# Performance work log

Measured on AMD Instinct MI355X. Metric: run time of the kernel, lower is better.

The kernel has to match this reference:

```python
import jax, jax.numpy as jnp
import numpy as np
from jax import lax

K2 = 3                 # support_kernel_size
TARGET_OCC = 0.5
OCC_W = 10.0
ITERS = 10             # flood-fill iterations
THRESH = 0.5
STEEP = 20.0

# 6-neighbor 3D cross kernel (plus-shaped), shape [O=1, I=1, 3, 3, 3]
_cross_np = np.zeros((1, 1, 3, 3, 3), dtype=np.float32)
for dz, dy, dx in [(0, 1, 1), (2, 1, 1), (1, 0, 1), (1, 2, 1), (1, 1, 0), (1, 1, 2)]:
    _cross_np[0, 0, dz, dy, dx] = 1.0


def _conv3d(x, k, pad):
    # x: [B, C, D, H, W], k: [O, I, kd, kh, kw]
    return lax.conv_general_dilated(
        x, k, window_strides=(1, 1, 1), padding=pad,
        dimension_numbers=('NCDHW', 'OIDHW', 'NCDHW'))


def setup_inputs() -> dict:
    key = jax.random.key(0)
    voxel_grid = jax.random.uniform(key, (4, 1, 128, 128, 128), dtype=jnp.float32)
    return {"voxel_grid": voxel_grid}


def reference(voxel_grid):
    B, C, D, H, W = voxel_grid.shape
    N = B * D * H * W
    dt = voxel_grid.dtype

    # ---- overhang score: vectorized over all z-slices at once ----
    # per-slice conv2d(3x3 ones) == conv3d with kernel depth 1
    k2 = jnp.ones((1, 1, 1, K2, K2), dt)
    below = voxel_grid[:, :, :-1]          # [B,1,D-1,H,W]
    curr = voxel_grid[:, :, 1:]
    below_support = _conv3d(below, k2, ((0, 0), (1, 1), (1, 1)))
    support_ratio = below_support / (K2 * K2)
    overhang = (curr * (1.0 - support_ratio)).sum() / N

    # ---- surface area score ----
    k3 = jnp.ones((1, 1, 3, 3, 3), dt)
    neighbor_solid = _conv3d(voxel_grid, k3, ((1, 1), (1, 1), (1, 1)))
    surface_term = neighbor_solid.sum() / 27.0 / N

    occupancy = voxel_grid.sum() / N
    occupancy_penalty = OCC_W * (occupancy - TARGET_OCC) ** 2

    # differentiable flood-fill (diff_find_enclosed_voids)
    seed = jnp.zeros_like(voxel_grid).at[:, :, 5, 5, 5].set(1.0)
    cross = jnp.asarray(_cross_np, dt)
    not_solid = 1.0 - voxel_grid

    def body(i, mask):
        c = _conv3d(mask, cross, ((1, 1), (1, 1), (1, 1)))
        act = jax.nn.sigmoid(STEEP * (c - THRESH))
        return jnp.maximum(mask, act) * not_solid

    enclosed = lax.fori_loop(0, ITERS, body, seed)
    resin_trap_penalty = 100.0 * enclosed.sum() / N

    surface_score = surface_term - resin_trap_penalty - occupancy_penalty
    return overhang, surface_score
```

## Files before the change

kernel.cpp:

```cpp
#include <hip/hip_runtime.h>

#define HW    (128*128)
#define DHW   (128*128*128)
#define NTOT  (4*DHW)
#define NBLK  2048

__device__ __forceinline__ float sigf(float x){ return 1.0f/(1.0f+__expf(-x)); }
__device__ __forceinline__ float4 ld4(const float* p){ return *(const float4*)p; }


__global__ __launch_bounds__(256, 4) void mega_k(
    const float* __restrict__ v, float* __restrict__ p_occ,
    float* __restrict__ p_surf, float* __restrict__ p_over,
    float* __restrict__ p_trap)
{
    __shared__ float4 smem4[1445];
    __shared__ float sred[16];
    float* smem = (float*)smem4;

    const int bid = blockIdx.x;
    const int tid = threadIdx.x;
    const float4 zero4 = make_float4(0,0,0,0);

    if (bid < 4) {
        const int b = bid;
        const size_t gb = (size_t)b * DHW;
        const int ty = tid & 15, tz = tid >> 4;
        const float a_lo = sigf(-10.0f), a_hi = sigf(10.0f);
        #define M(zz,yy) (smem + (((zz)*17 + (yy))*20))

        float m[16], nv[16];
        {
            const float* rv = v + gb + ((size_t)tz*128 + ty)*128;
            int dzy = abs(tz-5) + abs(ty-5);
            #pragma unroll
            for (int q = 0; q < 4; ++q) {
                int x4 = 4*q;
                float4 a = ld4(rv + x4);
                nv[x4+0]=1.f-a.x; nv[x4+1]=1.f-a.y; nv[x4+2]=1.f-a.z; nv[x4+3]=1.f-a.w;
                int d0=dzy+abs(x4+0-5), d1=dzy+abs(x4+1-5);
                int d2=dzy+abs(x4+2-5), d3=dzy+abs(x4+3-5);
                m[x4+0] = ((d0==0)?1.f:((d0==1)?a_hi:a_lo)) * nv[x4+0];
                m[x4+1] = ((d1==0)?1.f:((d1==1)?a_hi:a_lo)) * nv[x4+1];
                m[x4+2] = ((d2==0)?1.f:((d2==1)?a_hi:a_lo)) * nv[x4+2];
                m[x4+3] = ((d3==0)?1.f:((d3==1)?a_hi:a_lo)) * nv[x4+3];
                *(float4*)(M(tz,ty) + x4) = make_float4(m[x4+0],m[x4+1],m[x4+2],m[x4+3]);
            }
        }
        const float xrE = a_lo * (1.f - v[gb + ((size_t)tz*128 + ty)*128 + 16]);
        {
            int a = tid >> 4, e = tid & 15;
            M(16,a)[e] = a_lo * (1.f - v[gb + ((size_t)16*128 + a)*128 + e]);
            M(a,16)[e] = a_lo * (1.f - v[gb + ((size_t)a*128 + 16)*128 + e]);
        }
        __syncthreads();

        for (int it = 0; it < 9; ++it) {
            const float* YM = M(tz,ty-1);
            const float* YP = M(tz,ty+1);
            const float* ZM = M(tz-1,ty);
            const float* ZP = M(tz+1,ty);
            float nm[16];
            #pragma unroll
            for (int q = 0; q < 4; ++q) {
                int x4 = 4*q;
                float4 ym = (ty > 0) ? *(const float4*)(YM + x4) : zero4;
                float4 yp = *(const float4*)(YP + x4);
                float4 zm = (tz > 0) ? *(const float4*)(ZM + x4) : zero4;
                float4 zp = *(const float4*)(ZP + x4);
                float xl = (q == 0) ? 0.f : m[x4-1];
                float xr = (q == 3) ? xrE : m[x4+4];
                float s0 = xl      + m[x4+1] + ym.x + yp.x + zm.x + zp.x;
                float s1 = m[x4+0] + m[x4+2] + ym.y + yp.y + zm.y + zp.y;
                float s2 = m[x4+1] + m[x4+3] + ym.z + yp.z + zm.z + zp.z;
                float s3 = m[x4+2] + xr      + ym.w + yp.w + zm.w + zp.w;
                nm[x4+0] = fmaxf(m[x4+0], sigf(20.f*s0 - 10.f)) * nv[x4+0];
                nm[x4+1] = fmaxf(m[x4+1], sigf(20.f*s1 - 10.f)) * nv[x4+1];
                nm[x4+2] = fmaxf(m[x4+2], sigf(20.f*s2 - 10.f)) * nv[x4+2];
                nm[x4+3] = fmaxf(m[x4+3], sigf(20.f*s3 - 10.f)) * nv[x4+3];
            }
            __syncthreads();
            float* W = M(tz,ty);
            #pragma unroll
            for (int q = 0; q < 4; ++q) {
                int x4 = 4*q;
                *(float4*)(W + x4) = make_float4(nm[x4+0],nm[x4+1],nm[x4+2],nm[x4+3]);
                m[x4+0]=nm[x4+0]; m[x4+1]=nm[x4+1]; m[x4+2]=nm[x4+2]; m[x4+3]=nm[x4+3];
            }
            __syncthreads();
        }

        float d = 0.f;
        #pragma unroll
        for (int x = 0; x < 16; ++x) d += m[x] - a_lo * nv[x];
        #pragma unroll
        for (int o = 32; o; o >>= 1) d += __shfl_down(d, o, 64);
        int lane = tid & 63, wid = tid >> 6;
        if (lane == 0) sred[wid] = d;
        __syncthreads();
        if (tid == 0) p_trap[b] = sred[0] + sred[1] + sred[2] + sred[3];
        #undef M
    } else {
        const int rid = bid - 4;
        const int b   = rid >> 9;
        const int rem = rid & 511;
        const int z0  = (rem >> 4) * 4;
        const int y0  = (rem & 15) * 8;
        const int tx  = tid & 31, ty = tid >> 5;
        const int x4  = tx * 4;
        const int y   = y0 + ty;
        const size_t gb = (size_t)b * DHW;
        #define PB(p,r) (smem + ((p)*1320 + (r)*132))

        float occ = 0.f, surf = 0.f, over = 0.f;

        if (z0 >= 1) {
            const float* bp = v + gb + (size_t)(z0-1)*HW;
            for (int i = tid; i < 320; i += 256) {
                int r = i >> 5, xq = i & 31, xi = xq*4;
                int gy = y0 - 1 + r;
                float4 q = ((unsigned)gy <= 127u) ? ld4(bp + gy*128 + xi) : zero4;
                float ql = __shfl_up(q.w, 1);   if (xq == 0)  ql = 0.f;
                float qr = __shfl_down(q.x, 1); if (xq == 31) qr = 0.f;
                *(float4*)(PB(0,r) + xi) =
                    make_float4(ql+q.x+q.y, q.x+q.y+q.z, q.y+q.z+q.w, q.z+q.w+qr);
            }
        }
        __syncthreads();

        const float wy = (y==0 || y==127) ? 2.f : 3.f;
        const float wx0 = (x4==0)   ? 2.f : 3.f;
        const float wx3 = (x4==124) ? 2.f : 3.f;
        const float inv9 = 1.f/9.f;

        int pb = 0;
        for (int s = 0; s < 4; ++s) {
            const int z = z0 + s;
            const float* cp = v + gb + (size_t)z*HW;
            float4 val = ld4(cp + y*128 + x4);

            occ += val.x + val.y + val.z + val.w;
            float wz = (z==0 || z==127) ? 2.f : 3.f;
            surf += wz*wy*(wx0*val.x + 3.f*val.y + 3.f*val.z + wx3*val.w);

            if (z >= 1) {
                float4 a = *(const float4*)(PB(pb, ty)   + x4);
                float4 c = *(const float4*)(PB(pb, ty+1) + x4);
                float4 d = *(const float4*)(PB(pb, ty+2) + x4);
                float4 S = make_float4(a.x+c.x+d.x, a.y+c.y+d.y,
                                       a.z+c.z+d.z, a.w+c.w+d.w);
                over += val.x*(1.f - S.x*inv9) + val.y*(1.f - S.y*inv9)
                      + val.z*(1.f - S.z*inv9) + val.w*(1.f - S.w*inv9);
            }

            if (s < 3) {
                float ql = __shfl_up(val.w, 1);   if (tx == 0)  ql = 0.f;
                float qr = __shfl_down(val.x, 1); if (tx == 31) qr = 0.f;
                *(float4*)(PB(pb^1, ty+1) + x4) =
                    make_float4(ql+val.x+val.y, val.x+val.y+val.z,
                                val.y+val.z+val.w, val.z+val.w+qr);
                if (tid < 64) {
                    int h = tid >> 5, xq = tid & 31, xi = xq*4;
                    int gy = h ? (y0 + 8) : (y0 - 1);
                    float4 q = ((unsigned)gy <= 127u) ? ld4(cp + gy*128 + xi) : zero4;
                    float hl = __shfl_up(q.w, 1);   if (xq == 0)  hl = 0.f;
                    float hr = __shfl_down(q.x, 1); if (xq == 31) hr = 0.f;
                    *(float4*)(PB(pb^1, h*9) + xi) =
                        make_float4(hl+q.x+q.y, q.x+q.y+q.z, q.y+q.z+q.w, q.z+q.w+hr);
                }
                pb ^= 1;
            }
            __syncthreads();
        }

        #pragma unroll
        for (int o = 32; o; o >>= 1) {
            occ  += __shfl_down(occ,  o, 64);
            surf += __shfl_down(surf, o, 64);
            over += __shfl_down(over, o, 64);
        }
        int lane = tid & 63, wid = tid >> 6;
        if (lane == 0) { sred[wid]=occ; sred[4+wid]=surf; sred[8+wid]=over; }
        __syncthreads();
        if (tid == 0) {
            p_occ [rid] = sred[0]+sred[1]+sred[2]+sred[3];
            p_surf[rid] = sred[4]+sred[5]+sred[6]+sred[7];
            p_over[rid] = sred[8]+sred[9]+sred[10]+sred[11];
        }
        #undef PB
    }
}

__global__ __launch_bounds__(1024) void finalize_k(
    const float* __restrict__ p_occ, const float* __restrict__ p_surf,
    const float* __restrict__ p_over, const float* __restrict__ p_trap,
    float* __restrict__ out)
{
    double occ=0, surf=0, over=0;
    for (int i = threadIdx.x; i < NBLK; i += 1024) {
        occ += p_occ[i]; surf += p_surf[i]; over += p_over[i];
    }
    __shared__ double sm[3][16];
    #pragma unroll
    for (int o = 32; o; o >>= 1) {
        occ  += __shfl_down(occ,  o, 64);
        surf += __shfl_down(surf, o, 64);
        over += __shfl_down(over, o, 64);
    }
    int lane = threadIdx.x & 63, wid = threadIdx.x >> 6;
    if (lane == 0) { sm[0][wid]=occ; sm[1][wid]=surf; sm[2][wid]=over; }
    __syncthreads();
    if (threadIdx.x == 0) {
        double so=0, ss=0, sv=0;
        for (int w = 0; w < 16; ++w) { so+=sm[0][w]; ss+=sm[1][w]; sv+=sm[2][w]; }
        double dS = (double)p_trap[0] + p_trap[1] + p_trap[2] + p_trap[3];
        double a_lo = 1.0 / (1.0 + exp(10.0));
        double N = (double)NTOT;
        double trap_sum = a_lo * (N - so) + dS;
        double occupancy = so / N;
        double occ_pen = 10.0 * (occupancy - 0.5) * (occupancy - 0.5);
        out[0] = (float)(sv / N);
        out[1] = (float)(ss / 27.0 / N - 100.0 * trap_sum / N - occ_pen);
    }
}

extern "C" void kernel_launch(void* const* d_in, const int* in_sizes, int n_in,
                              void* d_out, int out_size, void* d_ws, size_t ws_size,
                              hipStream_t stream)
{
    const float* v = (const float*)d_in[0];
    float* out = (float*)d_out;
    float* ws = (float*)d_ws;

    float* p_occ  = ws;
    float* p_surf = p_occ  + NBLK;
    float* p_over = p_surf + NBLK;
    float* p_trap = p_over + NBLK;

    mega_k<<<NBLK + 4, 256, 0, stream>>>(v, p_occ, p_surf, p_over, p_trap);
    finalize_k<<<1, 1024, 0, stream>>>(p_occ, p_surf, p_over, p_trap, out);
}
```

Baseline: 84.49 us.

## Preload all z-slices and use four shared planes with a single barrier

The stats blocks now issue all four z-slice loads and every halo-row load at the start. The horizontally summed rows for each slice go into separate shared-memory planes instead of a double-buffered pair. This replaces the per-slice load, store and __syncthreads sequence with one barrier, which raises memory-level parallelism and cuts synchronization. It costs more shared memory and registers per block, which could lower occupancy, and it may not matter if the few flood-fill blocks set the kernel time.

Measured after the change: 85.01 us (median of 2 runs). About the same (+0.6%).

```diff
diff --git a/kernel.cpp b/kernel.cpp
--- a/kernel.cpp
+++ b/kernel.cpp
@@ -112,7 +112,10 @@
         const size_t gb = (size_t)b * DHW;
         #define PB(p,r) (smem + ((p)*1320 + (r)*132))
 
-        float occ = 0.f, surf = 0.f, over = 0.f;
+        float4 vals[4];
+        #pragma unroll
+        for (int s = 0; s < 4; ++s)
+            vals[s] = ld4(v + gb + (size_t)(z0+s)*HW + y*128 + x4);
 
         if (z0 >= 1) {
             const float* bp = v + gb + (size_t)(z0-1)*HW;
@@ -126,51 +129,50 @@
                     make_float4(ql+q.x+q.y, q.x+q.y+q.z, q.y+q.z+q.w, q.z+q.w+qr);
             }
         }
-        __syncthreads();
-
-        const float wy = (y==0 || y==127) ? 2.f : 3.f;
+        if (tid < 192) {
+            int ps = tid >> 6;
+            int r6 = tid & 63;
+            int h  = r6 >> 5, xq = r6 & 31, xi = xq*4;
+            int gy = h ? (y0 + 8) : (y0 - 1);
+            float4 q = ((unsigned)gy <= 127u)
+                     ? ld4(v + gb + (size_t)(z0+ps)*HW + gy*128 + xi) : zero4;
+            float hl = __shfl_up(q.w, 1);   if (xq == 0)  hl = 0.f;
+            float hr = __shfl_down(q.x, 1); if (xq == 31) hr = 0.f;
+            *(float4*)(PB(ps+1, h ? 9 : 0) + xi) =
+                make_float4(hl+q.x+q.y, q.x+q.y+q.z, q.y+q.z+q.w, q.z+q.w+hr);
+        }
+        #pragma unroll
+        for (int s = 0; s < 3; ++s) {
+            float4 q = vals[s];
+            float ql = __shfl_up(q.w, 1);   if (tx == 0)  ql = 0.f;
+            float qr = __shfl_down(q.x, 1); if (tx == 31) qr = 0.f;
+            *(float4*)(PB(s+1, ty+1) + x4) =
+                make_float4(ql+q.x+q.y, q.x+q.y+q.z, q.y+q.z+q.w, q.z+q.w+qr);
+        }
+        __syncthreads();
+
+        const float wy  = (y==0 || y==127) ? 2.f : 3.f;
         const float wx0 = (x4==0)   ? 2.f : 3.f;
         const float wx3 = (x4==124) ? 2.f : 3.f;
         const float inv9 = 1.f/9.f;
 
-        int pb = 0;
+        float occ = 0.f, surf = 0.f, over = 0.f;
+        #pragma unroll
         for (int s = 0; s < 4; ++s) {
             const int z = z0 + s;
-            const float* cp = v + gb + (size_t)z*HW;
-            float4 val = ld4(cp + y*128 + x4);
-
+            float4 val = vals[s];
             occ += val.x + val.y + val.z + val.w;
             float wz = (z==0 || z==127) ? 2.f : 3.f;
             surf += wz*wy*(wx0*val.x + 3.f*val.y + 3.f*val.z + wx3*val.w);
-
             if (z >= 1) {
-                float4 a = *(const float4*)(PB(pb, ty)   + x4);
-                float4 c = *(const float4*)(PB(pb, ty+1) + x4);
-                float4 d = *(const float4*)(PB(pb, ty+2) + x4);
-                float4 S = make_float4(a.x+c.x+d.x, a.y+c.y+d.y,
-                                       a.z+c.z+d.z, a.w+c.w+d.w);
-                over += val.x*(1.f - S.x*inv9) + val.y*(1.f - S.y*inv9)
-                      + val.z*(1.f - S.z*inv9) + val.w*(1.f - S.w*inv9);
-            }
-
-            if (s < 3) {
-                float ql = __shfl_up(val.w, 1);   if (tx == 0)  ql = 0.f;
-                float qr = __shfl_down(val.x, 1); if (tx == 31) qr = 0.f;
-                *(float4*)(PB(pb^1, ty+1) + x4) =
-                    make_float4(ql+val.x+val.y, val.x+val.y+val.z,
-                                val.y+val.z+val.w, val.z+val.w+qr);
-                if (tid < 64) {
-                    int h = tid >> 5, xq = tid & 31, xi = xq*4;
-                    int gy = h ? (y0 + 8) : (y0 - 1);
-                    float4 q = ((unsigned)gy <= 127u) ? ld4(cp + gy*128 + xi) : zero4;
-                    float hl = __shfl_up(q.w, 1);   if (xq == 0)  hl = 0.f;
-                    float hr = __shfl_down(q.x, 1); if (xq == 31) hr = 0.f;
-                    *(float4*)(PB(pb^1, h*9) + xi) =
-                        make_float4(hl+q.x+q.y, q.x+q.y+q.z, q.y+q.z+q.w, q.z+q.w+hr);
-                }
-                pb ^= 1;
-            }
-            __syncthreads();
+                float4 a = *(const float4*)(PB(s, ty)   + x4);
+                float4 c = *(const float4*)(PB(s, ty+1) + x4);
+                float4 d = *(const float4*)(PB(s, ty+2) + x4);
+                over += val.x*(1.f - (a.x+c.x+d.x)*inv9)
+                      + val.y*(1.f - (a.y+c.y+d.y)*inv9)
+                      + val.z*(1.f - (a.z+c.z+d.z)*inv9)
+                      + val.w*(1.f - (a.w+c.w+d.w)*inv9);
+            }
         }
 
         #pragma unroll
```
